# Kernel tuning notes

Measured on AMD Instinct MI355X. Metric: run time of the kernel, lower is better.

Reference implementation:

```python
import jax, jax.numpy as jnp
import numpy as np
from jax import lax

K_KNN = 20           # DGCNN default neighborhood size
SLOPE = 0.2          # LeakyReLU negative slope


def _leaky(x):
    return jnp.where(x >= 0, x, SLOPE * x)


def _knn(x, k):
    # x: [B, N, C] -> idx [B, N, k] of nearest neighbors (incl. self) in feature space
    xx = jnp.sum(x * x, axis=-1)                       # [B, N]
    d = xx[:, :, None] + xx[:, None, :] - 2.0 * jnp.einsum('bnc,bmc->bnm', x, x)
    return lax.top_k(-d, k)[1]                          # [B, N, k]


def _edge_conv(x, idx, w, b):
    # x: [B, N, C]; idx: [B, N, k]; w: [O, 2C]; b: [O]
    neigh = jax.vmap(lambda xt, i: xt[i])(x, idx)       # [B, N, k, C]
    center = jnp.broadcast_to(x[:, :, None, :], neigh.shape)
    feat = jnp.concatenate([neigh - center, center], axis=-1)  # [B, N, k, 2C]
    h = _leaky(jnp.einsum('bnkc,oc->bnko', feat, w) + b)
    return jnp.max(h, axis=2)                           # [B, N, O]


def setup_inputs() -> dict:
    key = jax.random.key(0)
    ks = jax.random.split(key, 20)
    B, N, J, KR = 4, 4096, 24, 4
    layers = [64, 128, 256]

    def w_init(k, o, i):
        return jax.random.normal(k, (o, i), jnp.float32) / np.sqrt(i)

    inp = {
        'V': jax.random.normal(ks[0], (B, N, 3), jnp.float32),
        'W': jax.random.uniform(ks[1], (B, J, N), jnp.float32),
        'skeletonOneRingIdx': jax.random.randint(ks[2], (B, J, KR), 0, J),
    }
    # geoNet edge-conv params (input channels per layer: 3, 64, 128 -> 2C inputs)
    inp['g1_w'] = w_init(ks[3], 64, 6);    inp['g1_b'] = jnp.zeros((64,), jnp.float32)
    inp['g2_w'] = w_init(ks[4], 128, 128); inp['g2_b'] = jnp.zeros((128,), jnp.float32)
    inp['g3_w'] = w_init(ks[5], 256, 256); inp['g3_b'] = jnp.zeros((256,), jnp.float32)
    # skeleton edge-conv params (inputs: 451 -> 902, 256 -> 512, 128 -> 256)
    inp['s1_w'] = w_init(ks[6], 256, 902); inp['s1_b'] = jnp.zeros((256,), jnp.float32)
    inp['s2_w'] = w_init(ks[7], 128, 512); inp['s2_b'] = jnp.zeros((128,), jnp.float32)
    inp['s3_w'] = w_init(ks[8], 64, 256);  inp['s3_b'] = jnp.zeros((64,), jnp.float32)
    # jointMLP 1x1 convs: 448 -> 512 -> 256 -> 3
    inp['m1_w'] = w_init(ks[9], 512, 448);  inp['m1_b'] = jnp.zeros((512,), jnp.float32)
    inp['m2_w'] = w_init(ks[10], 256, 512); inp['m2_b'] = jnp.zeros((256,), jnp.float32)
    inp['m3_w'] = w_init(ks[11], 3, 256);   inp['m3_b'] = jnp.zeros((3,), jnp.float32)
    return inp


def reference(V, W, skeletonOneRingIdx,
              g1_w, g1_b, g2_w, g2_b, g3_w, g3_b,
              s1_w, s1_b, s2_w, s2_b, s3_w, s3_b,
              m1_w, m1_b, m2_w, m2_b, m3_w, m3_b):
    # ---- geoNet: DGCNN with dynamic kNN, output cat([xyz, l1, l2, l3]) -> [B, N, 451]
    outs = [V]
    h = V
    for w, b in ((g1_w, g1_b), (g2_w, g2_b), (g3_w, g3_b)):
        idx = _knn(h, K_KNN)
        h = _edge_conv(h, idx, w, b)
        outs.append(h)
    feat = jnp.concatenate(outs, axis=-1)                # [B, N, 451]

    # ---- weighted pooling onto skeleton joints
    pooled = jnp.einsum('bjn,bnc->bjc', W, feat)
    pooled = pooled / (jnp.sum(W, axis=-1, keepdims=True) + 1e-5)  # [B, J, 451]

    # ---- skeleton edge convs with fixed one-ring idx
    v1 = _edge_conv(pooled, skeletonOneRingIdx, s1_w, s1_b)  # [B, J, 256]
    v2 = _edge_conv(v1, skeletonOneRingIdx, s2_w, s2_b)      # [B, J, 128]
    v3 = _edge_conv(v2, skeletonOneRingIdx, s3_w, s3_b)      # [B, J, 64]

    joints = jnp.concatenate([v1, v2, v3], axis=-1)          # [B, J, 448]
    h = _leaky(jnp.einsum('bjc,oc->bjo', joints, m1_w) + m1_b)
    h = _leaky(jnp.einsum('bjc,oc->bjo', h, m2_w) + m2_b)
    out = jnp.einsum('bjc,oc->bjo', h, m3_w) + m3_b          # [B, J, 3]
    return out
```

## Files before the change

### kernel.cpp

```cpp
#include <hip/hip_runtime.h>
#include <hip/hip_bf16.h>
#include <float.h>

#define B_   4
#define N_   4096
#define J_   24
#define KR_  4
#define KNN_ 20
#define SLOPE 0.2f
#define SLABN 64
#define NSLAB (N_ / SLABN)
#define NTILE 32
#define SCAPW 320
#define KSLACK 8u

typedef __attribute__((ext_vector_type(8))) short bf16x8;
typedef __attribute__((ext_vector_type(4))) float f32x4;

__global__ void k_norm(const float* __restrict__ h, float* __restrict__ xx, int C) {
    int i = blockIdx.x * blockDim.x + threadIdx.x;
    if (i >= B_ * N_) return;
    const float* hp = h + (size_t)i * C;
    float s = 0.f;
    for (int c = 0; c < C; ++c) { float v = hp[c]; s += v * v; }
    xx[i] = s;
}

__device__ __forceinline__ unsigned mapf(float f) {
    unsigned u = __float_as_uint(f);
    return (u & 0x80000000u) ? ~u : (u | 0x80000000u);
}
__device__ __forceinline__ unsigned key16(float f) {
    return mapf(f) >> 16;
}

__global__ void k_split(const float* __restrict__ h, unsigned short* __restrict__ hi,
                        unsigned short* __restrict__ lo, int total4) {
    int i = blockIdx.x * 256 + threadIdx.x;
    if (i >= total4) return;
    float4 v = ((const float4*)h)[i];
    ushort4 h4, l4;
    {
        unsigned u = __float_as_uint(v.x); h4.x = (unsigned short)(u >> 16);
        float r = v.x - __uint_as_float(u & 0xffff0000u); l4.x = (unsigned short)(__float_as_uint(r) >> 16);
    }
    {
        unsigned u = __float_as_uint(v.y); h4.y = (unsigned short)(u >> 16);
        float r = v.y - __uint_as_float(u & 0xffff0000u); l4.y = (unsigned short)(__float_as_uint(r) >> 16);
    }
    {
        unsigned u = __float_as_uint(v.z); h4.z = (unsigned short)(u >> 16);
        float r = v.z - __uint_as_float(u & 0xffff0000u); l4.z = (unsigned short)(__float_as_uint(r) >> 16);
    }
    {
        unsigned u = __float_as_uint(v.w); h4.w = (unsigned short)(u >> 16);
        float r = v.w - __uint_as_float(u & 0xffff0000u); l4.w = (unsigned short)(__float_as_uint(r) >> 16);
    }
    ((ushort4*)hi)[i] = h4;
    ((ushort4*)lo)[i] = l4;
}

__global__ __launch_bounds__(256) void k_dist(const unsigned short* __restrict__ Hi,
                                              const unsigned short* __restrict__ Lo,
                                              int C,
                                              const float* __restrict__ xxall,
                                              unsigned short* __restrict__ Dall, int b0) {
    __shared__ unsigned short tile[128][136];
    int b = b0 + blockIdx.y;
    const unsigned short* XH = Hi + (size_t)b * N_ * C;
    const unsigned short* XL = Lo + (size_t)b * N_ * C;
    const float* xxb = xxall + (size_t)b * N_;
    unsigned short* D = Dall + (size_t)blockIdx.y * N_ * N_;

    int t = blockIdx.x;
    int ti = 0;
    while (t >= NTILE - ti) { t -= NTILE - ti; ++ti; }
    int tj = ti + t;
    int row0 = ti * 128, col0 = tj * 128;
    int tid  = threadIdx.x;
    int wv   = tid >> 6, lane = tid & 63;
    int wr   = wv >> 1,  wc   = wv & 1;
    int rbase = row0 + wr * 64;
    int cbase = col0 + wc * 64;
    int lp    = lane & 15;
    int kgrp  = lane >> 4;

    f32x4 acc[4][4];
#pragma unroll
    for (int i = 0; i < 4; ++i)
#pragma unroll
        for (int j = 0; j < 4; ++j) acc[i][j] = (f32x4){0.f, 0.f, 0.f, 0.f};

    for (int ks = 0; ks < C; ks += 32) {
        int kb = ks + kgrp * 8;
        bf16x8 ah[4], al[4];
#pragma unroll
        for (int fi = 0; fi < 4; ++fi) {
            size_t ro = (size_t)(rbase + fi * 16 + lp) * C + kb;
            ah[fi] = *(const bf16x8*)(XH + ro);
            al[fi] = *(const bf16x8*)(XL + ro);
        }
#pragma unroll
        for (int fj = 0; fj < 4; ++fj) {
            size_t co = (size_t)(cbase + fj * 16 + lp) * C + kb;
            bf16x8 bh = *(const bf16x8*)(XH + co);
            bf16x8 bl = *(const bf16x8*)(XL + co);
#pragma unroll
            for (int fi = 0; fi < 4; ++fi) {
                acc[fi][fj] = __builtin_amdgcn_mfma_f32_16x16x32_bf16(ah[fi], bh, acc[fi][fj], 0, 0, 0);
                acc[fi][fj] = __builtin_amdgcn_mfma_f32_16x16x32_bf16(ah[fi], bl, acc[fi][fj], 0, 0, 0);
                acc[fi][fj] = __builtin_amdgcn_mfma_f32_16x16x32_bf16(al[fi], bh, acc[fi][fj], 0, 0, 0);
            }
        }
    }

    float xxrv = xxb[rbase + lane];
    float xxcv = xxb[cbase + lane];
    int rsub = (lane >> 4) * 4;
#pragma unroll
    for (int fi = 0; fi < 4; ++fi) {
#pragma unroll
        for (int fj = 0; fj < 4; ++fj) {
            float xc = __shfl(xxcv, fj * 16 + lp, 64);
#pragma unroll
            for (int r = 0; r < 4; ++r) {
                float xr = __shfl(xxrv, fi * 16 + rsub + r, 64);
                float d = xr + xc - 2.f * acc[fi][fj][r];
                tile[wr * 64 + fi * 16 + rsub + r][wc * 64 + fj * 16 + lp] =
                    (unsigned short)key16(d);
            }
        }
    }
    __syncthreads();

    {
        int r0   = tid >> 4;
        int cseg = (tid & 15) * 8;
#pragma unroll
        for (int q = 0; q < 8; ++q) {
            int row = r0 + q * 16;
            *(uint4*)(D + (size_t)(row0 + row) * N_ + col0 + cseg) =
                *(const uint4*)&tile[row][cseg];
        }
    }
    if (ti == tj) return;
    {
        int c0g = tid >> 4;
        int g   = tid & 15;
#pragma unroll
        for (int cq = 0; cq < 8; ++cq) {
            int c = c0g + cq * 16;
            unsigned short s[8];
#pragma unroll
            for (int q = 0; q < 8; ++q) s[q] = tile[g * 8 + q][c];
            *(uint4*)(D + (size_t)(col0 + c) * N_ + row0 + g * 8) = *(const uint4*)s;
        }
    }
}

__device__ __forceinline__ unsigned radixsel_wave(unsigned val, int r, int nbits) {
    unsigned long long cand = ~0ull;
    unsigned prefix = 0;
    for (int bit = nbits - 1; bit >= 0; --bit) {
        unsigned long long z = cand & __ballot(!((val >> bit) & 1u));
        int cz = __popcll(z);
        if (cz >= r) cand = z;
        else { r -= cz; cand &= ~z; prefix |= 1u << bit; }
    }
    return prefix;
}

__device__ __forceinline__ bool top20_round(unsigned long long key, bool active) {
    unsigned hi = (unsigned)(key >> 32);
    unsigned lo = (unsigned)key;
    unsigned long long amask = __ballot(active);
    int navail = __popcll(amask);
    if (navail <= KNN_) return active;
    int r = KNN_;
    unsigned long long cand = amask;
    unsigned prefix = 0;
    for (int bit = 31; bit >= 0; --bit) {
        unsigned long long z = cand & __ballot(!((hi >> bit) & 1u));
        int cz = __popcll(z);
        if (cz >= r) cand = z;
        else { r -= cz; cand &= ~z; prefix |= 1u << bit; }
    }
    unsigned long long c2 = __ballot(active && hi == prefix);
    unsigned p2 = 0;
    for (int bit = 11; bit >= 0; --bit) {
        unsigned long long z = c2 & __ballot(!((lo >> bit) & 1u));
        int cz = __popcll(z);
        if (cz >= r) c2 = z;
        else { r -= cz; c2 &= ~z; p2 |= 1u << bit; }
    }
    return active && (hi < prefix || (hi == prefix && lo <= p2));
}

__device__ __forceinline__ void final_top20(const unsigned long long* skey, int S,
                                            unsigned long long* wbuf,
                                            int lane, int* idxout, int obase) {
    unsigned long long key = (lane < S) ? skey[lane] : ~0ull;
    bool active = (lane < S);
    int consumed = (S < 64) ? S : 64;
    int nw = 0;
    for (;;) {
        bool win = top20_round(key, active);
        unsigned long long wb = __ballot(win);
        nw = __popcll(wb);
        int pos = __popcll(wb & ((1ull << lane) - 1ull));
        if (win) wbuf[pos] = key;
        if (consumed >= S) break;
        int src = consumed + lane - nw;
        key = (lane < nw) ? wbuf[lane] : ((src < S) ? skey[src] : ~0ull);
        active = (lane < nw) || (src >= consumed && src < S);
        consumed += 64 - nw;
    }
    if (lane < nw) {
        unsigned long long mine = wbuf[lane];
        int rank = 0;
        for (int i = 0; i < nw; ++i) rank += (wbuf[i] < mine);
        idxout[obase + rank] = (int)(unsigned)mine;
    }
}

__global__ __launch_bounds__(256) void k_sel(const unsigned short* __restrict__ Dall,
                                             const float* __restrict__ Xall, int C,
                                             const float* __restrict__ xxall,
                                             int* __restrict__ knnIdx, int b0) {
    __shared__ unsigned short sidx[4][SCAPW];
    __shared__ unsigned long long skey[4][SCAPW];
    __shared__ unsigned long long wbuf[4][24];
    __shared__ int scnt[4];
    int b = b0 + blockIdx.y;
    const unsigned short* Db = Dall + (size_t)blockIdx.y * N_ * N_;
    const float* Xb  = Xall + (size_t)b * N_ * C;
    const float* xxb = xxall + (size_t)b * N_;
    int* idxout = knnIdx + (size_t)b * N_ * KNN_;
    int wv   = threadIdx.x >> 6;
    int lane = threadIdx.x & 63;
    int ql   = blockIdx.x * 4 + wv;
    if (lane == 0) scnt[wv] = 0;

    const uint4* row = (const uint4*)(Db + (size_t)ql * N_);
    uint4 K[8];
#pragma unroll
    for (int q = 0; q < 8; ++q) K[q] = row[q * 64 + lane];

    unsigned mn = 0xffffu;
#pragma unroll
    for (int q = 0; q < 8; ++q) {
        const unsigned* w = (const unsigned*)&K[q];
#pragma unroll
        for (int h = 0; h < 4; ++h) {
            unsigned lo = w[h] & 0xffffu, hi = w[h] >> 16;
            mn = (lo < mn) ? lo : mn;
            mn = (hi < mn) ? hi : mn;
        }
    }
    unsigned tau = radixsel_wave(mn, KNN_, 16) + KSLACK;
    if (tau > 0xffffu) tau = 0xffffu;

    int nl = 0;
#pragma unroll
    for (int q = 0; q < 8; ++q) {
        const unsigned* w = (const unsigned*)&K[q];
#pragma unroll
        for (int h = 0; h < 4; ++h) {
            nl += ((w[h] & 0xffffu) <= tau);
            nl += ((w[h] >> 16) <= tau);
        }
    }
    int p = atomicAdd(&scnt[wv], nl);
#pragma unroll
    for (int q = 0; q < 8; ++q) {
        const unsigned* w = (const unsigned*)&K[q];
        int jb = (q * 64 + lane) * 8;
#pragma unroll
        for (int h = 0; h < 4; ++h) {
            if ((w[h] & 0xffffu) <= tau) { if (p < SCAPW) sidx[wv][p] = (unsigned short)(jb + 2 * h);     ++p; }
            if ((w[h] >> 16)     <= tau) { if (p < SCAPW) sidx[wv][p] = (unsigned short)(jb + 2 * h + 1); ++p; }
        }
    }
    int S = scnt[wv];
    if (S > SCAPW) S = SCAPW;

    float xxq = xxb[ql];
    const float4* xq4 = (const float4*)(Xb + (size_t)ql * C);
    for (int s = lane; s < S; s += 64) {
        int j = (int)sidx[wv][s];
        const float4* xj = (const float4*)(Xb + (size_t)j * C);
        float a0 = 0.f, a1 = 0.f, a2 = 0.f, a3 = 0.f;
        for (int c4 = 0; c4 < (C >> 2); ++c4) {
            float4 x = xj[c4]; float4 qv = xq4[c4];
            a0 = fmaf(qv.x, x.x, a0);
            a1 = fmaf(qv.y, x.y, a1);
            a2 = fmaf(qv.z, x.z, a2);
            a3 = fmaf(qv.w, x.w, a3);
        }
        float dot = (a0 + a1) + (a2 + a3);
        float d = xxq + xxb[j] - 2.f * dot;
        skey[wv][s] = ((unsigned long long)mapf(d) << 32) | (unsigned)j;
    }
    final_top20(skey[wv], S, wbuf[wv], lane, idxout, ql * KNN_);
}

__global__ __launch_bounds__(256) void k_selC3(const float* __restrict__ V,
                                               const float* __restrict__ xx,
                                               int* __restrict__ knnIdx) {
    __shared__ unsigned long long skey[4][SCAPW];
    __shared__ unsigned long long wbuf[4][24];
    __shared__ int scnt[4];
    int b    = blockIdx.y;
    const float* Xb  = V + (size_t)b * N_ * 3;
    const float* xxb = xx + (size_t)b * N_;
    int* idxout = knnIdx + (size_t)b * N_ * KNN_;
    int wv   = threadIdx.x >> 6;
    int lane = threadIdx.x & 63;
    int q    = blockIdx.x * 4 + wv;
    if (lane == 0) scnt[wv] = 0;

    float qx = Xb[q * 3], qy = Xb[q * 3 + 1], qz = Xb[q * 3 + 2];
    float xxq = xxb[q];

    unsigned kk[64];
#pragma unroll
    for (int cq = 0; cq < 4; ++cq) {
        int jb = (cq * 64 + lane) * 16;
        float pts[48];
        const float4* src = (const float4*)(Xb + (size_t)jb * 3);
#pragma unroll
        for (int t = 0; t < 12; ++t) ((float4*)pts)[t] = src[t];
#pragma unroll
        for (int t = 0; t < 16; ++t) {
            float dot = qx * pts[3 * t];
            dot = fmaf(qy, pts[3 * t + 1], dot);
            dot = fmaf(qz, pts[3 * t + 2], dot);
            float d = xxq + xxb[jb + t] - 2.f * dot;
            kk[cq * 16 + t] = mapf(d);
        }
    }

    unsigned mn = kk[0];
#pragma unroll
    for (int t = 1; t < 64; ++t) mn = (kk[t] < mn) ? kk[t] : mn;
    unsigned tau = radixsel_wave(mn, KNN_, 32);

    int nl = 0;
#pragma unroll
    for (int t = 0; t < 64; ++t) nl += (kk[t] <= tau);
    int p = atomicAdd(&scnt[wv], nl);
#pragma unroll
    for (int cq = 0; cq < 4; ++cq) {
        int jb = (cq * 64 + lane) * 16;
#pragma unroll
        for (int t = 0; t < 16; ++t) {
            if (kk[cq * 16 + t] <= tau) {
                if (p < SCAPW)
                    skey[wv][p] = ((unsigned long long)kk[cq * 16 + t] << 32) | (unsigned)(jb + t);
                ++p;
            }
        }
    }
    int S = scnt[wv];
    if (S > SCAPW) S = SCAPW;
    final_top20(skey[wv], S, wbuf[wv], lane, idxout, q * KNN_);
}

__device__ __forceinline__ void prepP_elem(const float* __restrict__ w,
                                           const float* __restrict__ bias,
                                           int C, int O, float* __restrict__ P,
                                           float* __restrict__ b2, int i) {
    int O2 = 2 * O;
    if (i < O2) b2[i] = (i < O) ? 0.f : bias[i - O];
    if (i >= C * O2) return;
    int k = i / O2, col = i % O2;
    float v;
    if (col < O) v = w[(size_t)col * 2 * C + k];
    else { int o = col - O; v = w[(size_t)o * 2 * C + C + k] - w[(size_t)o * 2 * C + k]; }
    P[i] = v;
}
__device__ __forceinline__ void transp_elem(const float* __restrict__ w, int O, int K,
                                            float* __restrict__ wT, int i) {
    if (i >= O * K) return;
    int k = i / O, o = i % O;
    wT[i] = w[(size_t)o * K + k];
}

__global__ void k_prepall(const float* g1w, const float* g1b,
                          const float* g2w, const float* g2b,
                          const float* g3w, const float* g3b,
                          const float* s1w, const float* s1b,
                          const float* s2w, const float* s2b,
                          const float* s3w, const float* s3b,
                          const float* m1w, const float* m2w, const float* m3w,
                          float* P1, float* P2, float* P3, float* P4, float* P5,
                          float* P6, float* P7, float* P8, float* P9,
                          float* bb1, float* bb2, float* bb3,
                          float* bb4, float* bb5, float* bb6) {
    int i = blockIdx.x * 256 + threadIdx.x;
    switch (blockIdx.y) {
        case 0: prepP_elem(g1w, g1b, 3,   64,  P1, bb1, i); break;
        case 1: prepP_elem(g2w, g2b, 64,  128, P2, bb2, i); break;
        case 2: prepP_elem(g3w, g3b, 128, 256, P3, bb3, i); break;
        case 3: prepP_elem(s1w, s1b, 451, 256, P4, bb4, i); break;
        case 4: prepP_elem(s2w, s2b, 256, 128, P5, bb5, i); break;
        case 5: prepP_elem(s3w, s3b, 128, 64,  P6, bb6, i); break;
        case 6: transp_elem(m1w, 512, 448, P7, i); break;
        case 7: transp_elem(m2w, 256, 512, P8, i); break;
        case 8: transp_elem(m3w, 3,   256, P9, i); break;
    }
}

__global__ __launch_bounds__(256) void k_gemm(const float* __restrict__ A, int lda,
                                              const float* __restrict__ Bm,
                                              float* __restrict__ Cm, int ldc,
                                              int M, int N, int K,
                                              const float* __restrict__ bias, int leaky) {
    __shared__ float As[16][68];
    __shared__ float Bs[16][68];
    int tid = threadIdx.x;
    int row0 = blockIdx.y * 64, col0 = blockIdx.x * 64;
    int tr = tid >> 4, tc = tid & 15;
    float acc[4][4] = {{0.f}};
    for (int kt = 0; kt < K; kt += 16) {
#pragma unroll
        for (int i = 0; i < 4; ++i) {
            int e = tid + 256 * i;
            int r = e >> 4, kk = e & 15;
            int gr = row0 + r, gk = kt + kk;
            float v = 0.f;
            if (gr < M && gk < K) v = A[(size_t)gr * lda + gk];
            As[kk][r] = v;
        }
#pragma unroll
        for (int i = 0; i < 4; ++i) {
            int e = tid + 256 * i;
            int kk = e >> 6, c = e & 63;
            int gk = kt + kk, gc = col0 + c;
            float v = 0.f;
            if (gk < K && gc < N) v = Bm[(size_t)gk * N + gc];
            Bs[kk][c] = v;
        }
        __syncthreads();
#pragma unroll
        for (int kk = 0; kk < 16; ++kk) {
            float a[4], bv[4];
            *(float4*)&a[0]  = *(const float4*)&As[kk][tr * 4];
            *(float4*)&bv[0] = *(const float4*)&Bs[kk][tc * 4];
#pragma unroll
            for (int i = 0; i < 4; ++i)
#pragma unroll
                for (int j = 0; j < 4; ++j) acc[i][j] += a[i] * bv[j];
        }
        __syncthreads();
    }
#pragma unroll
    for (int i = 0; i < 4; ++i) {
        int r = row0 + tr * 4 + i;
        if (r >= M) continue;
#pragma unroll
        for (int j = 0; j < 4; ++j) {
            int c = col0 + tc * 4 + j;
            if (c >= N) continue;
            float v = acc[i][j];
            if (bias) v += bias[c];
            if (leaky) v = v >= 0.f ? v : SLOPE * v;
            Cm[(size_t)r * ldc + c] = v;
        }
    }
}

__global__ __launch_bounds__(256) void k_sgemm(const float* __restrict__ A, int lda,
                                               const float* __restrict__ Bm,
                                               float* __restrict__ Cm, int ldc,
                                               int N, int K,
                                               const float* __restrict__ bias, int leaky) {
    extern __shared__ float Arow[];
    int r   = blockIdx.x;
    int c0  = blockIdx.y * 256;
    int tid = threadIdx.x;
    for (int k = tid; k < K; k += 256) Arow[k] = A[(size_t)r * lda + k];
    __syncthreads();
    int c = c0 + tid;
    if (c >= N) return;
    float acc = bias ? bias[c] : 0.f;
    for (int k = 0; k < K; ++k) acc += Arow[k] * Bm[(size_t)k * N + c];
    if (leaky) acc = acc >= 0.f ? acc : SLOPE * acc;
    Cm[(size_t)r * ldc + c] = acc;
}

__global__ void k_gathermax(const float* __restrict__ Y, int O, int R,
                            const int* __restrict__ idx, int kc,
                            float* __restrict__ out, int ldo, int ooff,
                            float* __restrict__ xxout) {
    extern __shared__ int sidx[];
    __shared__ float red[256];
    int br = blockIdx.x;
    int b  = br / R;
    int o  = threadIdx.x;
    if (o < kc) sidx[o] = idx[(size_t)br * kc + o];
    __syncthreads();
    int O2 = 2 * O;
    float z = Y[(size_t)br * O2 + O + o];
    float best = -FLT_MAX;
    for (int k = 0; k < kc; ++k) {
        int m = sidx[k];
        best = fmaxf(best, Y[(size_t)(b * R + m) * O2 + o]);
    }
    float r = z + best;
    r = r >= 0.f ? r : SLOPE * r;
    out[(size_t)br * ldo + ooff + o] = r;
    if (xxout) {
        red[o] = r * r;
        __syncthreads();
        for (int s = blockDim.x >> 1; s > 0; s >>= 1) {
            if (o < s) red[o] += red[o + s];
            __syncthreads();
        }
        if (o == 0) xxout[br] = red[0];
    }
}

__device__ __forceinline__ void chan_map(int b, int c,
                                         const float* Vf, const float* l1,
                                         const float* l2, const float* l3,
                                         const float*& p, int& st) {
    if (c < 3)        { st = 3;   p = Vf + (size_t)b * N_ * 3   + c; }
    else if (c < 67)  { st = 64;  p = l1 + (size_t)b * N_ * 64  + (c - 3); }
    else if (c < 195) { st = 128; p = l2 + (size_t)b * N_ * 128 + (c - 67); }
    else              { st = 256; p = l3 + (size_t)b * N_ * 256 + (c - 195); }
}

__global__ __launch_bounds__(256) void k_pool2(const float* __restrict__ Vf,
                                               const float* __restrict__ l1,
                                               const float* __restrict__ l2,
                                               const float* __restrict__ l3,
                                               const float* __restrict__ W,
                                               float* __restrict__ ppool,
                                               float* __restrict__ psw) {
    __shared__ float Wl[SLABN][J_];
    int blk  = blockIdx.x;
    int b    = blk / NSLAB, slab = blk % NSLAB;
    int n0   = slab * SLABN;
    int tid  = threadIdx.x;

    for (int e = tid; e < J_ * SLABN; e += 256) {
        int j = e / SLABN, n = e % SLABN;
        Wl[n][j] = W[((size_t)b * J_ + j) * N_ + n0 + n];
    }
    __syncthreads();

    if (tid < J_) {
        float s = 0.f;
        for (int n = 0; n < SLABN; ++n) s += Wl[n][tid];
        psw[(size_t)blk * J_ + tid] = s;
    }

    int c0 = tid, c1 = tid + 256;
    const float *p0, *p1 = nullptr; int s0, s1 = 0;
    chan_map(b, c0, Vf, l1, l2, l3, p0, s0);
    bool has1 = (c1 < 451);
    if (has1) chan_map(b, c1, Vf, l1, l2, l3, p1, s1);

    float acc0[J_], acc1[J_];
#pragma unroll
    for (int j = 0; j < J_; ++j) { acc0[j] = 0.f; acc1[j] = 0.f; }

    for (int n = 0; n < SLABN; ++n) {
        float v0 = p0[(size_t)(n0 + n) * s0];
        float v1 = has1 ? p1[(size_t)(n0 + n) * s1] : 0.f;
        const float* wn = &Wl[n][0];
#pragma unroll
        for (int q = 0; q < J_ / 4; ++q) {
            float4 w4 = *(const float4*)(wn + 4 * q);
            acc0[4*q+0] += w4.x * v0;  acc1[4*q+0] += w4.x * v1;
            acc0[4*q+1] += w4.y * v0;  acc1[4*q+1] += w4.y * v1;
            acc0[4*q+2] += w4.z * v0;  acc1[4*q+2] += w4.z * v1;
            acc0[4*q+3] += w4.w * v0;  acc1[4*q+3] += w4.w * v1;
        }
    }
    float* pp = ppool + (size_t)blk * J_ * 451;
#pragma unroll
    for (int j = 0; j < J_; ++j) {
        pp[(size_t)j * 451 + c0] = acc0[j];
        if (has1) pp[(size_t)j * 451 + c1] = acc1[j];
    }
}

__global__ __launch_bounds__(256) void k_poolred(const float* __restrict__ ppool,
                                                 const float* __restrict__ psw,
                                                 float* __restrict__ pooled) {
    int bj = blockIdx.x;
    int b  = bj / J_, j = bj % J_;
    int tid = threadIdx.x;

    float sw = 0.f;
    for (int sl = 0; sl < NSLAB; ++sl) sw += psw[(size_t)(b * NSLAB + sl) * J_ + j];
    float inv = 1.f / (sw + 1e-5f);

    for (int c = tid; c < 451; c += 256) {
        float s = 0.f;
        for (int sl = 0; sl < NSLAB; ++sl)
            s += ppool[((size_t)(b * NSLAB + sl) * J_ + j) * 451 + c];
        pooled[(size_t)bj * 451 + c] = s * inv;
    }
}

extern "C" void kernel_launch(void* const* d_in, const int* in_sizes, int n_in,
                              void* d_out, int out_size, void* d_ws, size_t ws_size,
                              hipStream_t stream) {
    const float* V  = (const float*)d_in[0];
    const float* W  = (const float*)d_in[1];
    const int* ringIdx = (const int*)d_in[2];
    const float* g1w = (const float*)d_in[3];
    const float* g1b = (const float*)d_in[4];
    const float* g2w = (const float*)d_in[5];
    const float* g2b = (const float*)d_in[6];
    const float* g3w = (const float*)d_in[7];
    const float* g3b = (const float*)d_in[8];
    const float* s1w = (const float*)d_in[9];
    const float* s1b = (const float*)d_in[10];
    const float* s2w = (const float*)d_in[11];
    const float* s2b = (const float*)d_in[12];
    const float* s3w = (const float*)d_in[13];
    const float* s3b = (const float*)d_in[14];
    const float* m1w = (const float*)d_in[15];
    const float* m1b = (const float*)d_in[16];
    const float* m2w = (const float*)d_in[17];
    const float* m2b = (const float*)d_in[18];
    const float* m3w = (const float*)d_in[19];
    const float* m3b = (const float*)d_in[20];
    (void)n_in; (void)in_sizes; (void)out_size;

    const int szP1 = 3 * 128,    szP2 = 64 * 256,  szP3 = 128 * 512;
    const int szP4 = 451 * 512,  szP5 = 256 * 256, szP6 = 128 * 128;
    const int szP7 = 448 * 512,  szP8 = 512 * 256, szP9 = 256 * 3;

    auto dreg_floats = [&](int nd) -> size_t {
        size_t a = (size_t)nd * ((size_t)N_ * N_ / 2);
        size_t ymax = (size_t)B_ * N_ * 512;
        size_t pool = (size_t)B_ * NSLAB * J_ * 451 + (size_t)B_ * NSLAB * J_;
        size_t r = a;
        if (ymax > r) r = ymax;
        if (pool > r) r = pool;
        return r;
    };
    auto layout_bytes = [&](int nd) -> size_t {
        size_t f = 0;
        f += (size_t)B_ * N_ * 64 + (size_t)B_ * N_ * 128 + (size_t)B_ * N_ * 256;
        f += (size_t)B_ * N_;
        f += dreg_floats(nd);
        f += 2 * ((size_t)B_ * N_ * 128 / 2);
        f += (size_t)B_ * N_ * KNN_;
        f += (size_t)B_ * J_ * 451 + (size_t)B_ * J_ * 448;
        f += (size_t)B_ * J_ * 512 + (size_t)B_ * J_ * 256;
        f += (size_t)(szP1 + szP2 + szP3 + szP4 + szP5 + szP6 + szP7 + szP8 + szP9);
        f += 128 + 256 + 512 + 512 + 256 + 128;
        return f * 4;
    };
    int nb = 1;
    if (ws_size >= layout_bytes(4)) nb = 4;
    else if (ws_size >= layout_bytes(2)) nb = 2;

    float* ws = (float*)d_ws;
    size_t off = 0;
    float* l1 = ws + off; off += (size_t)B_ * N_ * 64;
    float* l2 = ws + off; off += (size_t)B_ * N_ * 128;
    float* l3 = ws + off; off += (size_t)B_ * N_ * 256;
    float* xx = ws + off; off += (size_t)B_ * N_;
    float* D  = ws + off; off += dreg_floats(nb);
    unsigned short* Dk = (unsigned short*)D;
    float* Y  = D;
    float* ppool = D;
    float* psw   = D + (size_t)B_ * NSLAB * J_ * 451;
    unsigned short* Xhi = (unsigned short*)(ws + off); off += (size_t)B_ * N_ * 128 / 2;
    unsigned short* Xlo = (unsigned short*)(ws + off); off += (size_t)B_ * N_ * 128 / 2;
    int* knnIdx = (int*)(ws + off); off += (size_t)B_ * N_ * KNN_;
    float* pooled = ws + off; off += (size_t)B_ * J_ * 451;
    float* joints = ws + off; off += (size_t)B_ * J_ * 448;
    float* h1 = ws + off; off += (size_t)B_ * J_ * 512;
    float* h2 = ws + off; off += (size_t)B_ * J_ * 256;
    float* P1 = ws + off; off += szP1;
    float* P2 = ws + off; off += szP2;
    float* P3 = ws + off; off += szP3;
    float* P4 = ws + off; off += szP4;
    float* P5 = ws + off; off += szP5;
    float* P6 = ws + off; off += szP6;
    float* P7 = ws + off; off += szP7;
    float* P8 = ws + off; off += szP8;
    float* P9 = ws + off; off += szP9;
    float* bb1 = ws + off; off += 128;
    float* bb2 = ws + off; off += 256;
    float* bb3 = ws + off; off += 512;
    float* bb4 = ws + off; off += 512;
    float* bb5 = ws + off; off += 256;
    float* bb6 = ws + off; off += 128;

    const int M = B_ * N_;
    const int MJ = B_ * J_;
    const int NUTRI = NTILE * (NTILE + 1) / 2;

    k_prepall<<<dim3((szP4 + 255) / 256, 9), 256, 0, stream>>>(
        g1w, g1b, g2w, g2b, g3w, g3b, s1w, s1b, s2w, s2b, s3w, s3b,
        m1w, m2w, m3w, P1, P2, P3, P4, P5, P6, P7, P8, P9,
        bb1, bb2, bb3, bb4, bb5, bb6);

    k_norm<<<(M + 255) / 256, 256, 0, stream>>>(V, xx, 3);
    k_selC3<<<dim3(N_ / 4, B_), 256, 0, stream>>>(V, xx, knnIdx);
    k_gemm<<<dim3(2, M / 64), 256, 0, stream>>>(V, 3, P1, Y, 128, M, 128, 3, bb1, 0);
    k_gathermax<<<M, 64, KNN_ * sizeof(int), stream>>>(Y, 64, N_, knnIdx, KNN_, l1, 64, 0, xx);

    k_split<<<(M * 64 / 4 + 255) / 256, 256, 0, stream>>>(l1, Xhi, Xlo, M * 64 / 4);
    for (int g = 0; g < B_; g += nb) {
        k_dist<<<dim3(NUTRI, nb), 256, 0, stream>>>(Xhi, Xlo, 64, xx, Dk, g);
        k_sel<<<dim3(N_ / 4, nb), 256, 0, stream>>>(Dk, l1, 64, xx, knnIdx, g);
    }
    k_gemm<<<dim3(4, M / 64), 256, 0, stream>>>(l1, 64, P2, Y, 256, M, 256, 64, bb2, 0);
    k_gathermax<<<M, 128, KNN_ * sizeof(int), stream>>>(Y, 128, N_, knnIdx, KNN_, l2, 128, 0, xx);

    k_split<<<(M * 128 / 4 + 255) / 256, 256, 0, stream>>>(l2, Xhi, Xlo, M * 128 / 4);
    for (int g = 0; g < B_; g += nb) {
        k_dist<<<dim3(NUTRI, nb), 256, 0, stream>>>(Xhi, Xlo, 128, xx, Dk, g);
        k_sel<<<dim3(N_ / 4, nb), 256, 0, stream>>>(Dk, l2, 128, xx, knnIdx, g);
    }
    k_gemm<<<dim3(8, M / 64), 256, 0, stream>>>(l2, 128, P3, Y, 512, M, 512, 128, bb3, 0);
    k_gathermax<<<M, 256, KNN_ * sizeof(int), stream>>>(Y, 256, N_, knnIdx, KNN_, l3, 256, 0, nullptr);

    k_pool2<<<B_ * NSLAB, 256, 0, stream>>>(V, l1, l2, l3, W, ppool, psw);
    k_poolred<<<MJ, 256, 0, stream>>>(ppool, psw, pooled);

    k_sgemm<<<dim3(MJ, 2), 256, 451 * sizeof(float), stream>>>(pooled, 451, P4, Y, 512, 512, 451, bb4, 0);
    k_gathermax<<<MJ, 256, KR_ * sizeof(int), stream>>>(Y, 256, J_, ringIdx, KR_, joints, 448, 0, nullptr);

    k_sgemm<<<dim3(MJ, 1), 256, 256 * sizeof(float), stream>>>(joints, 448, P5, Y, 256, 256, 256, bb5, 0);
    k_gathermax<<<MJ, 128, KR_ * sizeof(int), stream>>>(Y, 128, J_, ringIdx, KR_, joints, 448, 256, nullptr);

    k_sgemm<<<dim3(MJ, 1), 256, 128 * sizeof(float), stream>>>(joints + 256, 448, P6, Y, 128, 128, 128, bb6, 0);
    k_gathermax<<<MJ, 64, KR_ * sizeof(int), stream>>>(Y, 64, J_, ringIdx, KR_, joints, 448, 384, nullptr);

    k_sgemm<<<dim3(MJ, 2), 256, 448 * sizeof(float), stream>>>(joints, 448, P7, h1, 512, 512, 448, m1b, 1);
    k_sgemm<<<dim3(MJ, 1), 256, 512 * sizeof(float), stream>>>(h1, 512, P8, h2, 256, 256, 512, m2b, 1);
    k_sgemm<<<dim3(MJ, 1), 256, 256 * sizeof(float), stream>>>(h2, 256, P9, (float*)d_out, 3, 3, 256, m3b, 0);
}
```

Measured before the change: 841.2 us.

## Fuse kNN distance tiles with streaming top-k selection, dropping the NxN distance matrix

Replaces the separate distance kernel (which wrote a full NxN 16-bit key matrix per batch) and the selection kernel with one fused kernel. Each block owns 64 query rows and streams 256-column tiles computed with bf16 split MFMA. Candidates under a running threshold go into per-row shared buffers, which are re-pruned with a multi-key radix select at fixed iterations. This removes the large global write and reread of distance keys and the per-batch launch loop. The cost is that the symmetric triangular tiling is lost, so the dot products are computed twice. It also uses heavy shared memory, which lowers occupancy, and candidates past FS_CAP can be silently dropped.

```diff
diff --git a/kernel.cpp b/kernel.cpp
--- a/kernel.cpp
+++ b/kernel.cpp
@@ -10,8 +10,8 @@
 #define SLOPE 0.2f
 #define SLABN 64
 #define NSLAB (N_ / SLABN)
-#define NTILE 32
 #define SCAPW 320
+#define FS_CAP 160
 #define KSLACK 8u
 
 typedef __attribute__((ext_vector_type(8))) short bf16x8;
@@ -60,104 +60,6 @@
     ((ushort4*)lo)[i] = l4;
 }
 
-__global__ __launch_bounds__(256) void k_dist(const unsigned short* __restrict__ Hi,
-                                              const unsigned short* __restrict__ Lo,
-                                              int C,
-                                              const float* __restrict__ xxall,
-                                              unsigned short* __restrict__ Dall, int b0) {
-    __shared__ unsigned short tile[128][136];
-    int b = b0 + blockIdx.y;
-    const unsigned short* XH = Hi + (size_t)b * N_ * C;
-    const unsigned short* XL = Lo + (size_t)b * N_ * C;
-    const float* xxb = xxall + (size_t)b * N_;
-    unsigned short* D = Dall + (size_t)blockIdx.y * N_ * N_;
-
-    int t = blockIdx.x;
-    int ti = 0;
-    while (t >= NTILE - ti) { t -= NTILE - ti; ++ti; }
-    int tj = ti + t;
-    int row0 = ti * 128, col0 = tj * 128;
-    int tid  = threadIdx.x;
-    int wv   = tid >> 6, lane = tid & 63;
-    int wr   = wv >> 1,  wc   = wv & 1;
-    int rbase = row0 + wr * 64;
-    int cbase = col0 + wc * 64;
-    int lp    = lane & 15;
-    int kgrp  = lane >> 4;
-
-    f32x4 acc[4][4];
-#pragma unroll
-    for (int i = 0; i < 4; ++i)
-#pragma unroll
-        for (int j = 0; j < 4; ++j) acc[i][j] = (f32x4){0.f, 0.f, 0.f, 0.f};
-
-    for (int ks = 0; ks < C; ks += 32) {
-        int kb = ks + kgrp * 8;
-        bf16x8 ah[4], al[4];
-#pragma unroll
-        for (int fi = 0; fi < 4; ++fi) {
-            size_t ro = (size_t)(rbase + fi * 16 + lp) * C + kb;
-            ah[fi] = *(const bf16x8*)(XH + ro);
-            al[fi] = *(const bf16x8*)(XL + ro);
-        }
-#pragma unroll
-        for (int fj = 0; fj < 4; ++fj) {
-            size_t co = (size_t)(cbase + fj * 16 + lp) * C + kb;
-            bf16x8 bh = *(const bf16x8*)(XH + co);
-            bf16x8 bl = *(const bf16x8*)(XL + co);
-#pragma unroll
-            for (int fi = 0; fi < 4; ++fi) {
-                acc[fi][fj] = __builtin_amdgcn_mfma_f32_16x16x32_bf16(ah[fi], bh, acc[fi][fj], 0, 0, 0);
-                acc[fi][fj] = __builtin_amdgcn_mfma_f32_16x16x32_bf16(ah[fi], bl, acc[fi][fj], 0, 0, 0);
-                acc[fi][fj] = __builtin_amdgcn_mfma_f32_16x16x32_bf16(al[fi], bh, acc[fi][fj], 0, 0, 0);
-            }
-        }
-    }
-
-    float xxrv = xxb[rbase + lane];
-    float xxcv = xxb[cbase + lane];
-    int rsub = (lane >> 4) * 4;
-#pragma unroll
-    for (int fi = 0; fi < 4; ++fi) {
-#pragma unroll
-        for (int fj = 0; fj < 4; ++fj) {
-            float xc = __shfl(xxcv, fj * 16 + lp, 64);
-#pragma unroll
-            for (int r = 0; r < 4; ++r) {
-                float xr = __shfl(xxrv, fi * 16 + rsub + r, 64);
-                float d = xr + xc - 2.f * acc[fi][fj][r];
-                tile[wr * 64 + fi * 16 + rsub + r][wc * 64 + fj * 16 + lp] =
-                    (unsigned short)key16(d);
-            }
-        }
-    }
-    __syncthreads();
-
-    {
-        int r0   = tid >> 4;
-        int cseg = (tid & 15) * 8;
-#pragma unroll
-        for (int q = 0; q < 8; ++q) {
-            int row = r0 + q * 16;
-            *(uint4*)(D + (size_t)(row0 + row) * N_ + col0 + cseg) =
-                *(const uint4*)&tile[row][cseg];
-        }
-    }
-    if (ti == tj) return;
-    {
-        int c0g = tid >> 4;
-        int g   = tid & 15;
-#pragma unroll
-        for (int cq = 0; cq < 8; ++cq) {
-            int c = c0g + cq * 16;
-            unsigned short s[8];
-#pragma unroll
-            for (int q = 0; q < 8; ++q) s[q] = tile[g * 8 + q][c];
-            *(uint4*)(D + (size_t)(col0 + c) * N_ + row0 + g * 8) = *(const uint4*)s;
-        }
-    }
-}
-
 __device__ __forceinline__ unsigned radixsel_wave(unsigned val, int r, int nbits) {
     unsigned long long cand = ~0ull;
     unsigned prefix = 0;
@@ -166,6 +68,29 @@
         int cz = __popcll(z);
         if (cz >= r) cand = z;
         else { r -= cz; cand &= ~z; prefix |= 1u << bit; }
+    }
+    return prefix;
+}
+
+__device__ __forceinline__ unsigned radixsel_multi16(const unsigned short* keys,
+                                                     int S, int lane, int r) {
+    unsigned k0 = 0, k1 = 0, k2 = 0;
+    unsigned act = 0;
+    if (lane < S)        { k0 = keys[lane];        act |= 1u; }
+    if (lane + 64 < S)   { k1 = keys[lane + 64];   act |= 2u; }
+    if (lane + 128 < S)  { k2 = keys[lane + 128];  act |= 4u; }
+    unsigned prefix = 0;
+    for (int bit = 15; bit >= 0; --bit) {
+        unsigned zm = 0; int c = 0;
+        if ((act & 1u) && !((k0 >> bit) & 1u)) { zm |= 1u; ++c; }
+        if ((act & 2u) && !((k1 >> bit) & 1u)) { zm |= 2u; ++c; }
+        if ((act & 4u) && !((k2 >> bit) & 1u)) { zm |= 4u; ++c; }
+        unsigned long long b0 = __ballot(c >= 1);
+        unsigned long long b1 = __ballot(c >= 2);
+        unsigned long long b2 = __ballot(c >= 3);
+        int tot = __popcll(b0) + __popcll(b1) + __popcll(b2);
+        if (tot >= r) act = zm;
+        else { r -= tot; act &= ~zm; prefix |= 1u << bit; }
     }
     return prefix;
 }
@@ -223,85 +148,194 @@
     }
 }
 
-__global__ __launch_bounds__(256) void k_sel(const unsigned short* __restrict__ Dall,
-                                             const float* __restrict__ Xall, int C,
-                                             const float* __restrict__ xxall,
-                                             int* __restrict__ knnIdx, int b0) {
-    __shared__ unsigned short sidx[4][SCAPW];
-    __shared__ unsigned long long skey[4][SCAPW];
+__global__ __launch_bounds__(256) void k_distsel(const unsigned short* __restrict__ Hi,
+                                                 const unsigned short* __restrict__ Lo,
+                                                 int C,
+                                                 const float* __restrict__ Xall,
+                                                 const float* __restrict__ xxall,
+                                                 int* __restrict__ knnIdx) {
+    __shared__ unsigned short tile[64][256];
+    __shared__ unsigned short kbuf[64][FS_CAP];
+    __shared__ unsigned short cbuf[64][FS_CAP];
+    __shared__ unsigned long long skey2[4][FS_CAP];
     __shared__ unsigned long long wbuf[4][24];
-    __shared__ int scnt[4];
-    int b = b0 + blockIdx.y;
-    const unsigned short* Db = Dall + (size_t)blockIdx.y * N_ * N_;
+    __shared__ unsigned tauA[64];
+    __shared__ int scntA[64];
+
+    int b = blockIdx.y;
+    const unsigned short* XH = Hi + (size_t)b * N_ * C;
+    const unsigned short* XL = Lo + (size_t)b * N_ * C;
     const float* Xb  = Xall + (size_t)b * N_ * C;
     const float* xxb = xxall + (size_t)b * N_;
     int* idxout = knnIdx + (size_t)b * N_ * KNN_;
-    int wv   = threadIdx.x >> 6;
-    int lane = threadIdx.x & 63;
-    int ql   = blockIdx.x * 4 + wv;
-    if (lane == 0) scnt[wv] = 0;
-
-    const uint4* row = (const uint4*)(Db + (size_t)ql * N_);
-    uint4 K[8];
-#pragma unroll
-    for (int q = 0; q < 8; ++q) K[q] = row[q * 64 + lane];
-
-    unsigned mn = 0xffffu;
-#pragma unroll
-    for (int q = 0; q < 8; ++q) {
-        const unsigned* w = (const unsigned*)&K[q];
-#pragma unroll
-        for (int h = 0; h < 4; ++h) {
-            unsigned lo = w[h] & 0xffffu, hi = w[h] >> 16;
-            mn = (lo < mn) ? lo : mn;
-            mn = (hi < mn) ? hi : mn;
-        }
-    }
-    unsigned tau = radixsel_wave(mn, KNN_, 16) + KSLACK;
-    if (tau > 0xffffu) tau = 0xffffu;
-
-    int nl = 0;
-#pragma unroll
-    for (int q = 0; q < 8; ++q) {
-        const unsigned* w = (const unsigned*)&K[q];
-#pragma unroll
-        for (int h = 0; h < 4; ++h) {
-            nl += ((w[h] & 0xffffu) <= tau);
-            nl += ((w[h] >> 16) <= tau);
-        }
-    }
-    int p = atomicAdd(&scnt[wv], nl);
-#pragma unroll
-    for (int q = 0; q < 8; ++q) {
-        const unsigned* w = (const unsigned*)&K[q];
-        int jb = (q * 64 + lane) * 8;
-#pragma unroll
-        for (int h = 0; h < 4; ++h) {
-            if ((w[h] & 0xffffu) <= tau) { if (p < SCAPW) sidx[wv][p] = (unsigned short)(jb + 2 * h);     ++p; }
-            if ((w[h] >> 16)     <= tau) { if (p < SCAPW) sidx[wv][p] = (unsigned short)(jb + 2 * h + 1); ++p; }
-        }
-    }
-    int S = scnt[wv];
-    if (S > SCAPW) S = SCAPW;
-
-    float xxq = xxb[ql];
-    const float4* xq4 = (const float4*)(Xb + (size_t)ql * C);
-    for (int s = lane; s < S; s += 64) {
-        int j = (int)sidx[wv][s];
-        const float4* xj = (const float4*)(Xb + (size_t)j * C);
-        float a0 = 0.f, a1 = 0.f, a2 = 0.f, a3 = 0.f;
-        for (int c4 = 0; c4 < (C >> 2); ++c4) {
-            float4 x = xj[c4]; float4 qv = xq4[c4];
-            a0 = fmaf(qv.x, x.x, a0);
-            a1 = fmaf(qv.y, x.y, a1);
-            a2 = fmaf(qv.z, x.z, a2);
-            a3 = fmaf(qv.w, x.w, a3);
-        }
-        float dot = (a0 + a1) + (a2 + a3);
-        float d = xxq + xxb[j] - 2.f * dot;
-        skey[wv][s] = ((unsigned long long)mapf(d) << 32) | (unsigned)j;
-    }
-    final_top20(skey[wv], S, wbuf[wv], lane, idxout, ql * KNN_);
+    int R0 = blockIdx.x * 64;
+    int tid = threadIdx.x, wv = tid >> 6, lane = tid & 63;
+    int lp = lane & 15, kgrp = lane >> 4, rsub = (lane >> 4) * 4;
+    int cwoff = wv * 64;
+    unsigned long long lmaskLT = (1ull << lane) - 1ull;
+
+    float xxrv = xxb[R0 + lane];
+
+    for (int it = 0; it < 16; ++it) {
+        int cb0 = it * 256 + cwoff;
+        f32x4 acc[4][4];
+#pragma unroll
+        for (int i = 0; i < 4; ++i)
+#pragma unroll
+            for (int j = 0; j < 4; ++j) acc[i][j] = (f32x4){0.f, 0.f, 0.f, 0.f};
+        for (int ks = 0; ks < C; ks += 32) {
+            int kb = ks + kgrp * 8;
+            bf16x8 ah[4], al[4];
+#pragma unroll
+            for (int fi = 0; fi < 4; ++fi) {
+                size_t ro = (size_t)(R0 + fi * 16 + lp) * C + kb;
+                ah[fi] = *(const bf16x8*)(XH + ro);
+                al[fi] = *(const bf16x8*)(XL + ro);
+            }
+#pragma unroll
+            for (int fj = 0; fj < 4; ++fj) {
+                size_t co = (size_t)(cb0 + fj * 16 + lp) * C + kb;
+                bf16x8 bh = *(const bf16x8*)(XH + co);
+                bf16x8 bl = *(const bf16x8*)(XL + co);
+#pragma unroll
+                for (int fi = 0; fi < 4; ++fi) {
+                    acc[fi][fj] = __builtin_amdgcn_mfma_f32_16x16x32_bf16(ah[fi], bh, acc[fi][fj], 0, 0, 0);
+                    acc[fi][fj] = __builtin_amdgcn_mfma_f32_16x16x32_bf16(ah[fi], bl, acc[fi][fj], 0, 0, 0);
+                    acc[fi][fj] = __builtin_amdgcn_mfma_f32_16x16x32_bf16(al[fi], bh, acc[fi][fj], 0, 0, 0);
+                }
+            }
+        }
+        float xxcv = xxb[cb0 + lane];
+#pragma unroll
+        for (int fi = 0; fi < 4; ++fi) {
+#pragma unroll
+            for (int fj = 0; fj < 4; ++fj) {
+                float xc = __shfl(xxcv, fj * 16 + lp, 64);
+#pragma unroll
+                for (int r = 0; r < 4; ++r) {
+                    float xr = __shfl(xxrv, fi * 16 + rsub + r, 64);
+                    float d = xr + xc - 2.f * acc[fi][fj][r];
+                    int row = fi * 16 + rsub + r;
+                    int col = cwoff + fj * 16 + lp;
+                    int pg = (col >> 3) ^ ((row >> 2) & 31);
+                    tile[row][(pg << 3) | (col & 7)] = (unsigned short)key16(d);
+                }
+            }
+        }
+        __syncthreads();
+        for (int rr = 0; rr < 16; ++rr) {
+            int row = (wv << 4) + rr;
+            int pg = (lane >> 1) ^ ((row >> 2) & 31);
+            const unsigned* kp = (const unsigned*)&tile[row][(pg << 3) | ((lane & 1) << 2)];
+            unsigned w0 = kp[0], w1 = kp[1];
+            unsigned k4[4];
+            k4[0] = w0 & 0xffffu; k4[1] = w0 >> 16;
+            k4[2] = w1 & 0xffffu; k4[3] = w1 >> 16;
+            unsigned mn4 = k4[0];
+            mn4 = (k4[1] < mn4) ? k4[1] : mn4;
+            mn4 = (k4[2] < mn4) ? k4[2] : mn4;
+            mn4 = (k4[3] < mn4) ? k4[3] : mn4;
+
+            unsigned tau;
+            int scnt = 0;
+            bool doApp;
+            if (it == 0) {
+                tau = radixsel_wave(mn4, KNN_, 16) + KSLACK;
+                if (tau > 0xffffu) tau = 0xffffu;
+                doApp = true;
+            } else {
+                tau = tauA[row];
+                doApp = (__ballot(mn4 <= tau) != 0ull);
+                if (doApp) scnt = scntA[row];
+            }
+            if (doApp) {
+                int gc = it * 256 + (lane << 2);
+#pragma unroll
+                for (int t = 0; t < 4; ++t) {
+                    bool in = (k4[t] <= tau);
+                    unsigned long long m = __ballot(in);
+                    int pos = scnt + __popcll(m & lmaskLT);
+                    if (in && pos < FS_CAP) {
+                        kbuf[row][pos] = (unsigned short)k4[t];
+                        cbuf[row][pos] = (unsigned short)(gc + t);
+                    }
+                    scnt += __popcll(m);
+                }
+                if (scnt > FS_CAP) scnt = FS_CAP;
+                if (lane == 0) {
+                    scntA[row] = scnt;
+                    if (it == 0) tauA[row] = tau;
+                }
+            }
+            if (it == 2 || it == 7) {
+                int S = scntA[row];
+                unsigned t2 = radixsel_multi16(&kbuf[row][0], S, lane, KNN_) + KSLACK;
+                if (t2 > 0xffffu) t2 = 0xffffu;
+                int S2 = 0;
+                for (int base = 0; base < S; base += 64) {
+                    int si = base + lane;
+                    unsigned kk = 0, cc = 0; bool in = false;
+                    if (si < S) {
+                        kk = kbuf[row][si]; cc = cbuf[row][si];
+                        in = (kk <= t2);
+                    }
+                    unsigned long long m = __ballot(in);
+                    int pos = S2 + __popcll(m & lmaskLT);
+                    if (in) {
+                        kbuf[row][pos] = (unsigned short)kk;
+                        cbuf[row][pos] = (unsigned short)cc;
+                    }
+                    S2 += __popcll(m);
+                }
+                if (lane == 0) { scntA[row] = S2; tauA[row] = t2; }
+            }
+        }
+        __syncthreads();
+    }
+
+    for (int rr = 0; rr < 16; ++rr) {
+        int row = (wv << 4) + rr;
+        int grow = R0 + row;
+        int S = scntA[row]; if (S > FS_CAP) S = FS_CAP;
+        float xxq = xxb[grow];
+        const float4* xq4 = (const float4*)(Xb + (size_t)grow * C);
+        unsigned myk[3] = {0xffffffffu, 0xffffffffu, 0xffffffffu};
+        unsigned myc[3] = {0u, 0u, 0u};
+        unsigned mn = 0xffffffffu;
+#pragma unroll
+        for (int ch = 0; ch < 3; ++ch) {
+            int s = lane + (ch << 6);
+            if (s < S) {
+                int j = (int)cbuf[row][s];
+                const float4* xj = (const float4*)(Xb + (size_t)j * C);
+                float a0 = 0.f, a1 = 0.f, a2 = 0.f, a3 = 0.f;
+                for (int c4 = 0; c4 < (C >> 2); ++c4) {
+                    float4 x = xj[c4]; float4 qv = xq4[c4];
+                    a0 = fmaf(qv.x, x.x, a0);
+                    a1 = fmaf(qv.y, x.y, a1);
+                    a2 = fmaf(qv.z, x.z, a2);
+                    a3 = fmaf(qv.w, x.w, a3);
+                }
+                float d = xxq + xxb[j] - 2.f * ((a0 + a1) + (a2 + a3));
+                unsigned k = mapf(d);
+                myk[ch] = k; myc[ch] = (unsigned)j;
+                mn = (k < mn) ? k : mn;
+            }
+        }
+        unsigned tau3 = radixsel_wave(mn, KNN_, 32);
+        int nch = (S + 63) >> 6;
+        int S2 = 0;
+#pragma unroll
+        for (int ch = 0; ch < 3; ++ch) {
+            if (ch >= nch) break;
+            bool in = (lane + (ch << 6) < S) && (myk[ch] <= tau3);
+            unsigned long long m = __ballot(in);
+            int pos = S2 + __popcll(m & lmaskLT);
+            if (in) skey2[wv][pos] = ((unsigned long long)myk[ch] << 32) | myc[ch];
+            S2 += __popcll(m);
+        }
+        final_top20(skey2[wv], S2, wbuf[wv], lane, idxout, grow * KNN_);
+    }
 }
 
 __global__ __launch_bounds__(256) void k_selC3(const float* __restrict__ V,
@@ -630,37 +664,15 @@
     const float* m2b = (const float*)d_in[18];
     const float* m3w = (const float*)d_in[19];
     const float* m3b = (const float*)d_in[20];
-    (void)n_in; (void)in_sizes; (void)out_size;
+    (void)n_in; (void)in_sizes; (void)out_size; (void)ws_size;
 
     const int szP1 = 3 * 128,    szP2 = 64 * 256,  szP3 = 128 * 512;
     const int szP4 = 451 * 512,  szP5 = 256 * 256, szP6 = 128 * 128;
     const int szP7 = 448 * 512,  szP8 = 512 * 256, szP9 = 256 * 3;
 
-    auto dreg_floats = [&](int nd) -> size_t {
-        size_t a = (size_t)nd * ((size_t)N_ * N_ / 2);
-        size_t ymax = (size_t)B_ * N_ * 512;
-        size_t pool = (size_t)B_ * NSLAB * J_ * 451 + (size_t)B_ * NSLAB * J_;
-        size_t r = a;
-        if (ymax > r) r = ymax;
-        if (pool > r) r = pool;
-        return r;
-    };
-    auto layout_bytes = [&](int nd) -> size_t {
-        size_t f = 0;
-        f += (size_t)B_ * N_ * 64 + (size_t)B_ * N_ * 128 + (size_t)B_ * N_ * 256;
-        f += (size_t)B_ * N_;
-        f += dreg_floats(nd);
-        f += 2 * ((size_t)B_ * N_ * 128 / 2);
-        f += (size_t)B_ * N_ * KNN_;
-        f += (size_t)B_ * J_ * 451 + (size_t)B_ * J_ * 448;
-        f += (size_t)B_ * J_ * 512 + (size_t)B_ * J_ * 256;
-        f += (size_t)(szP1 + szP2 + szP3 + szP4 + szP5 + szP6 + szP7 + szP8 + szP9);
-        f += 128 + 256 + 512 + 512 + 256 + 128;
-        return f * 4;
-    };
-    int nb = 1;
-    if (ws_size >= layout_bytes(4)) nb = 4;
-    else if (ws_size >= layout_bytes(2)) nb = 2;
+    size_t ymax = (size_t)B_ * N_ * 512;
+    size_t pool = (size_t)B_ * NSLAB * J_ * 451 + (size_t)B_ * NSLAB * J_;
+    size_t dreg = (ymax > pool) ? ymax : pool;
 
     float* ws = (float*)d_ws;
     size_t off = 0;
@@ -668,11 +680,9 @@
     float* l2 = ws + off; off += (size_t)B_ * N_ * 128;
     float* l3 = ws + off; off += (size_t)B_ * N_ * 256;
     float* xx = ws + off; off += (size_t)B_ * N_;
-    float* D  = ws + off; off += dreg_floats(nb);
-    unsigned short* Dk = (unsigned short*)D;
-    float* Y  = D;
-    float* ppool = D;
-    float* psw   = D + (size_t)B_ * NSLAB * J_ * 451;
+    float* Y  = ws + off; off += dreg;
+    float* ppool = Y;
+    float* psw   = Y + (size_t)B_ * NSLAB * J_ * 451;
     unsigned short* Xhi = (unsigned short*)(ws + off); off += (size_t)B_ * N_ * 128 / 2;
     unsigned short* Xlo = (unsigned short*)(ws + off); off += (size_t)B_ * N_ * 128 / 2;
     int* knnIdx = (int*)(ws + off); off += (size_t)B_ * N_ * KNN_;
@@ -698,7 +708,6 @@
 
     const int M = B_ * N_;
     const int MJ = B_ * J_;
-    const int NUTRI = NTILE * (NTILE + 1) / 2;
 
     k_prepall<<<dim3((szP4 + 255) / 256, 9), 256, 0, stream>>>(
         g1w, g1b, g2w, g2b, g3w, g3b, s1w, s1b, s2w, s2b, s3w, s3b,
@@ -711,18 +720,12 @@
     k_gathermax<<<M, 64, KNN_ * sizeof(int), stream>>>(Y, 64, N_, knnIdx, KNN_, l1, 64, 0, xx);
 
     k_split<<<(M * 64 / 4 + 255) / 256, 256, 0, stream>>>(l1, Xhi, Xlo, M * 64 / 4);
-    for (int g = 0; g < B_; g += nb) {
-        k_dist<<<dim3(NUTRI, nb), 256, 0, stream>>>(Xhi, Xlo, 64, xx, Dk, g);
-        k_sel<<<dim3(N_ / 4, nb), 256, 0, stream>>>(Dk, l1, 64, xx, knnIdx, g);
-    }
+    k_distsel<<<dim3(N_ / 64, B_), 256, 0, stream>>>(Xhi, Xlo, 64, l1, xx, knnIdx);
     k_gemm<<<dim3(4, M / 64), 256, 0, stream>>>(l1, 64, P2, Y, 256, M, 256, 64, bb2, 0);
     k_gathermax<<<M, 128, KNN_ * sizeof(int), stream>>>(Y, 128, N_, knnIdx, KNN_, l2, 128, 0, xx);
 
     k_split<<<(M * 128 / 4 + 255) / 256, 256, 0, stream>>>(l2, Xhi, Xlo, M * 128 / 4);
-    for (int g = 0; g < B_; g += nb) {
-        k_dist<<<dim3(NUTRI, nb), 256, 0, stream>>>(Xhi, Xlo, 128, xx, Dk, g);
-        k_sel<<<dim3(N_ / 4, nb), 256, 0, stream>>>(Dk, l2, 128, xx, knnIdx, g);
-    }
+    k_distsel<<<dim3(N_ / 64, B_), 256, 0, stream>>>(Xhi, Xlo, 128, l2, xx, knnIdx);
     k_gemm<<<dim3(8, M / 64), 256, 0, stream>>>(l2, 128, P3, Y, 512, M, 512, 128, bb3, 0);
     k_gathermax<<<M, 256, KNN_ * sizeof(int), stream>>>(Y, 256, N_, knnIdx, KNN_, l3, 256, 0, nullptr);
 
```

Result: slower. 1.313 ms (+56.1%).
